# Kernel tuning notes

Hardware: AMD Instinct MI355X
Metric: run time of the kernel (lower is better)

The kernel has to match this reference:

```python
import jax, jax.numpy as jnp
import numpy as np

N = 8192
F_IN = 256
F_OUT = 256
EDGE_P = 0.005  # graph density, avg degree ~41


def setup_inputs() -> dict:
    key = jax.random.key(0)
    k_x, k_adj, k_w, k_phi = jax.random.split(key, 4)
    x = jax.random.normal(k_x, (N, F_IN), dtype=jnp.float32)
    adj = (jax.random.uniform(k_adj, (N, N)) < EDGE_P).astype(jnp.float32)
    stdv_w = 1.0 / np.sqrt(F_OUT)  # torch uses weight.size(1)
    weight = jax.random.uniform(k_w, (F_IN, F_OUT), minval=-stdv_w, maxval=stdv_w, dtype=jnp.float32)
    bias = jnp.zeros((F_OUT,), dtype=jnp.float32)
    stdv_phi = 1.0  # 1/sqrt(phi.size(1)=1)
    phi = jax.random.uniform(k_phi, (2 * F_OUT, 1), minval=-stdv_phi, maxval=stdv_phi, dtype=jnp.float32)
    return {"adj": adj, "x": x, "weight": weight, "bias": bias, "phi": phi}


def reference(adj, x, weight, bias, phi):
    n = x.shape[0]
    H = x @ weight + bias  # [N, F]
    # S[i,j] = phi^T [H_i ; H_j] -> additive decomposition, no [N*N, 2F] concat
    f = H.shape[1]
    s_src = H @ phi[:f, 0]  # [N], contribution of row node i
    s_dst = H @ phi[f:, 0]  # [N], contribution of col node j
    S = s_src[:, None] + s_dst[None, :]  # [N, N]
    mask = (adj + jnp.eye(n, dtype=adj.dtype)) != 0
    S_masked = jnp.where(mask, S, -jnp.inf)
    attn = jax.nn.softmax(S_masked, axis=1)  # diag always unmasked -> no nan rows
    h = attn @ H  # [N, F]
    return jax.nn.leaky_relu(h, negative_slope=0.01)
```

## Files before the change

### kernel.cpp

```cpp
#include <hip/hip_runtime.h>
#include <hip/hip_bf16.h>

typedef __attribute__((ext_vector_type(8))) short short8;
typedef __attribute__((ext_vector_type(4))) float f32x4;

#define N_NODES 8192
#define F 256

static __device__ __forceinline__ unsigned short f2bf(float f) {
    unsigned int u = __builtin_bit_cast(unsigned int, f);
    u += 0x7FFFu + ((u >> 16) & 1u);
    return (unsigned short)(u >> 16);
}
static __device__ __forceinline__ float bf2f(unsigned short h) {
    unsigned int u = ((unsigned int)h) << 16;
    return __builtin_bit_cast(float, u);
}

__global__ __launch_bounds__(256) void k_prep(const float* __restrict__ W,
                                              unsigned short* __restrict__ Wt) {
    int k = blockIdx.x;
    int n = threadIdx.x;
    Wt[n * 256 + k] = f2bf(W[k * 256 + n]);
}

__global__ __launch_bounds__(256) void k_gemm(const float* __restrict__ x,
                                              const float* __restrict__ bias,
                                              const float* __restrict__ phi,
                                              const unsigned short* __restrict__ Wt,
                                              unsigned short* __restrict__ H,
                                              float* __restrict__ s_dst) {
    const int tid  = threadIdx.x;
    const int wave = tid >> 6;
    const int lane = tid & 63;
    const int lrow = lane & 15;
    const int lk   = lane >> 4;
    const int r0   = blockIdx.x * 64 + wave * 16;

    f32x4 acc[16];
#pragma unroll
    for (int n = 0; n < 16; ++n) acc[n] = (f32x4){0.f, 0.f, 0.f, 0.f};

#pragma unroll
    for (int k0 = 0; k0 < 256; k0 += 32) {
        const float* ap = x + (size_t)(r0 + lrow) * 256 + k0 + lk * 8;
        float4 a0 = *(const float4*)ap;
        float4 a1 = *(const float4*)(ap + 4);
        short8 a;
        a[0] = (short)f2bf(a0.x); a[1] = (short)f2bf(a0.y);
        a[2] = (short)f2bf(a0.z); a[3] = (short)f2bf(a0.w);
        a[4] = (short)f2bf(a1.x); a[5] = (short)f2bf(a1.y);
        a[6] = (short)f2bf(a1.z); a[7] = (short)f2bf(a1.w);
#pragma unroll
        for (int n = 0; n < 16; ++n) {
            short8 b = *(const short8*)(Wt + (size_t)(n * 16 + lrow) * 256 + k0 + lk * 8);
            acc[n] = __builtin_amdgcn_mfma_f32_16x16x32_bf16(a, b, acc[n], 0, 0, 0);
        }
    }

    float sd[4] = {0.f, 0.f, 0.f, 0.f};
#pragma unroll
    for (int n = 0; n < 16; ++n) {
        int c = n * 16 + lrow;
        float bv = bias[c];
        float ph = phi[256 + c];
#pragma unroll
        for (int i = 0; i < 4; ++i) {
            int r = r0 + lk * 4 + i;
            float h = acc[n][i] + bv;
            H[(size_t)r * 256 + c] = f2bf(h);
            sd[i] += h * ph;
        }
    }
#pragma unroll
    for (int m = 1; m < 16; m <<= 1) {
#pragma unroll
        for (int i = 0; i < 4; ++i) sd[i] += __shfl_xor(sd[i], m, 64);
    }
    if (lrow == 0) {
#pragma unroll
        for (int i = 0; i < 4; ++i) s_dst[r0 + lk * 4 + i] = sd[i];
    }
}

#define CAP 256
__global__ __launch_bounds__(256) void k_attn(const float* __restrict__ adj,
                                              const unsigned short* __restrict__ H,
                                              const float* __restrict__ s_dst,
                                              float* __restrict__ out) {
    __shared__ int   s_idx[4][CAP];
    __shared__ float s_w[4][CAP];
    __shared__ int   s_cnt[4];

    const int tid  = threadIdx.x;
    const int wave = tid >> 6;
    const int lane = tid & 63;
    const int i    = (blockIdx.x << 2) | wave;

    if (lane == 0) s_cnt[wave] = 0;
    __syncthreads();

    const float4* __restrict__ arow = (const float4*)(adj + (size_t)i * N_NODES);
#pragma unroll 4
    for (int c = 0; c < 32; ++c) {
        int v4 = (c << 6) | lane;
        float4 v = arow[v4];
        int col = v4 << 2;
        float vv[4] = {v.x, v.y, v.z, v.w};
        bool act[4];
        bool any = false;
#pragma unroll
        for (int j = 0; j < 4; ++j) {
            act[j] = (vv[j] != 0.f) || ((col + j) == i);
            any |= act[j];
        }
        if (any) {
#pragma unroll
            for (int j = 0; j < 4; ++j) {
                if (act[j]) {
                    int p = atomicAdd(&s_cnt[wave], 1);
                    if (p < CAP) s_idx[wave][p] = col + j;
                }
            }
        }
    }
    int cnt = min(s_cnt[wave], CAP);

    float mv = -3e38f;
    for (int t = lane; t < cnt; t += 64) {
        float sv = s_dst[s_idx[wave][t]];
        s_w[wave][t] = sv;
        mv = fmaxf(mv, sv);
    }
#pragma unroll
    for (int d = 32; d; d >>= 1) mv = fmaxf(mv, __shfl_xor(mv, d, 64));

    float zv = 0.f;
    for (int t = lane; t < cnt; t += 64) {
        float w = __expf(s_w[wave][t] - mv);
        s_w[wave][t] = w;
        zv += w;
    }
#pragma unroll
    for (int d = 32; d; d >>= 1) zv += __shfl_xor(zv, d, 64);
    const float zinv = 1.0f / zv;

    float a0 = 0.f, a1 = 0.f, a2 = 0.f, a3 = 0.f;
    const unsigned short* __restrict__ hb = H + (lane << 2);
#pragma unroll 4
    for (int t = 0; t < cnt; ++t) {
        int   j = s_idx[wave][t];
        float w = s_w[wave][t];
        short4 hv = *(const short4*)(hb + (size_t)j * F);
        a0 = fmaf(w, bf2f((unsigned short)hv.x), a0);
        a1 = fmaf(w, bf2f((unsigned short)hv.y), a1);
        a2 = fmaf(w, bf2f((unsigned short)hv.z), a2);
        a3 = fmaf(w, bf2f((unsigned short)hv.w), a3);
    }
    float4 o;
    o.x = a0 * zinv; o.y = a1 * zinv; o.z = a2 * zinv; o.w = a3 * zinv;
    o.x = (o.x >= 0.f) ? o.x : 0.01f * o.x;
    o.y = (o.y >= 0.f) ? o.y : 0.01f * o.y;
    o.z = (o.z >= 0.f) ? o.z : 0.01f * o.z;
    o.w = (o.w >= 0.f) ? o.w : 0.01f * o.w;
    *(float4*)(out + (size_t)i * F + (lane << 2)) = o;
}

extern "C" void kernel_launch(void* const* d_in, const int* in_sizes, int n_in,
                              void* d_out, int out_size, void* d_ws, size_t ws_size,
                              hipStream_t stream) {
    const float* adj  = (const float*)d_in[0];
    const float* x    = (const float*)d_in[1];
    const float* W    = (const float*)d_in[2];
    const float* bias = (const float*)d_in[3];
    const float* phi  = (const float*)d_in[4];
    float* out = (float*)d_out;

    char* ws = (char*)d_ws;
    unsigned short* Wt = (unsigned short*)ws;
    unsigned short* H  = (unsigned short*)(ws + (131072));
    float* s_dst       = (float*)(ws + 131072 + 4194304);

    hipLaunchKernelGGL(k_prep, dim3(256),          dim3(256), 0, stream, W, Wt);
    hipLaunchKernelGGL(k_gemm, dim3(N_NODES / 64), dim3(256), 0, stream,
                       x, bias, phi, Wt, H, s_dst);
    hipLaunchKernelGGL(k_attn, dim3(N_NODES / 4),  dim3(256), 0, stream,
                       adj, H, s_dst, out);
}
```

Before: 399.7 us.

## Replace LDS atomic neighbor compaction with ballot prefix and unroll padded gather

Neighbor compaction in the attention kernel now uses wave ballots and mbcnt prefix counts instead of per-element shared-memory atomics, and adjacency rows are read with nontemporal loads. Index and weight are packed into one int2 in shared memory, and the gather loop is padded to a multiple of eight with zero-weight entries so it can be fully unrolled for more outstanding H loads. The CAP overflow guard is dropped, so rows with more than 256 neighbors would write out of bounds.

After: 378.9 us. -5.2%, faster.

```diff
diff --git a/kernel.cpp b/kernel.cpp
--- a/kernel.cpp
+++ b/kernel.cpp
@@ -6,6 +6,7 @@
 
 #define N_NODES 8192
 #define F 256
+#define CAP 256
 
 static __device__ __forceinline__ unsigned short f2bf(float f) {
     unsigned int u = __builtin_bit_cast(unsigned int, f);
@@ -83,79 +84,102 @@
     }
 }
 
-#define CAP 256
 __global__ __launch_bounds__(256) void k_attn(const float* __restrict__ adj,
                                               const unsigned short* __restrict__ H,
                                               const float* __restrict__ s_dst,
                                               float* __restrict__ out) {
-    __shared__ int   s_idx[4][CAP];
-    __shared__ float s_w[4][CAP];
-    __shared__ int   s_cnt[4];
+    __shared__ int  s_idx[4][CAP];
+    __shared__ int2 s_pk[4][CAP];
 
     const int tid  = threadIdx.x;
     const int wave = tid >> 6;
     const int lane = tid & 63;
     const int i    = (blockIdx.x << 2) | wave;
 
-    if (lane == 0) s_cnt[wave] = 0;
-    __syncthreads();
-
-    const float4* __restrict__ arow = (const float4*)(adj + (size_t)i * N_NODES);
-#pragma unroll 4
+    const f32x4* __restrict__ arow = (const f32x4*)(adj + (size_t)i * N_NODES);
+    int cnt = 0;
+#pragma unroll 8
     for (int c = 0; c < 32; ++c) {
         int v4 = (c << 6) | lane;
-        float4 v = arow[v4];
+        f32x4 v = __builtin_nontemporal_load(arow + v4);
         int col = v4 << 2;
-        float vv[4] = {v.x, v.y, v.z, v.w};
-        bool act[4];
-        bool any = false;
-#pragma unroll
-        for (int j = 0; j < 4; ++j) {
-            act[j] = (vv[j] != 0.f) || ((col + j) == i);
-            any |= act[j];
-        }
-        if (any) {
-#pragma unroll
-            for (int j = 0; j < 4; ++j) {
-                if (act[j]) {
-                    int p = atomicAdd(&s_cnt[wave], 1);
-                    if (p < CAP) s_idx[wave][p] = col + j;
-                }
-            }
-        }
-    }
-    int cnt = min(s_cnt[wave], CAP);
+        bool a0 = (v[0] != 0.f) || (col + 0 == i);
+        bool a1 = (v[1] != 0.f) || (col + 1 == i);
+        bool a2 = (v[2] != 0.f) || (col + 2 == i);
+        bool a3 = (v[3] != 0.f) || (col + 3 == i);
+        unsigned long long b0 = __ballot(a0);
+        unsigned long long b1 = __ballot(a1);
+        unsigned long long b2 = __ballot(a2);
+        unsigned long long b3 = __ballot(a3);
+        int base = cnt;
+        if (a0) {
+            int off = __builtin_amdgcn_mbcnt_hi((unsigned)(b0 >> 32),
+                      __builtin_amdgcn_mbcnt_lo((unsigned)b0, 0u));
+            s_idx[wave][base + off] = col;
+        }
+        base += (int)__popcll(b0);
+        if (a1) {
+            int off = __builtin_amdgcn_mbcnt_hi((unsigned)(b1 >> 32),
+                      __builtin_amdgcn_mbcnt_lo((unsigned)b1, 0u));
+            s_idx[wave][base + off] = col + 1;
+        }
+        base += (int)__popcll(b1);
+        if (a2) {
+            int off = __builtin_amdgcn_mbcnt_hi((unsigned)(b2 >> 32),
+                      __builtin_amdgcn_mbcnt_lo((unsigned)b2, 0u));
+            s_idx[wave][base + off] = col + 2;
+        }
+        base += (int)__popcll(b2);
+        if (a3) {
+            int off = __builtin_amdgcn_mbcnt_hi((unsigned)(b3 >> 32),
+                      __builtin_amdgcn_mbcnt_lo((unsigned)b3, 0u));
+            s_idx[wave][base + off] = col + 3;
+        }
+        base += (int)__popcll(b3);
+        cnt = base;
+    }
+    asm volatile("s_waitcnt lgkmcnt(0)" ::: "memory");
 
     float mv = -3e38f;
     for (int t = lane; t < cnt; t += 64) {
-        float sv = s_dst[s_idx[wave][t]];
-        s_w[wave][t] = sv;
+        int j = s_idx[wave][t];
+        float sv = s_dst[j];
+        s_pk[wave][t].x = j;
+        s_pk[wave][t].y = __float_as_int(sv);
         mv = fmaxf(mv, sv);
     }
 #pragma unroll
     for (int d = 32; d; d >>= 1) mv = fmaxf(mv, __shfl_xor(mv, d, 64));
+    asm volatile("s_waitcnt lgkmcnt(0)" ::: "memory");
 
     float zv = 0.f;
     for (int t = lane; t < cnt; t += 64) {
-        float w = __expf(s_w[wave][t] - mv);
-        s_w[wave][t] = w;
+        int2 e = s_pk[wave][t];
+        float w = __expf(__int_as_float(e.y) - mv);
+        s_pk[wave][t].y = __float_as_int(w);
         zv += w;
     }
 #pragma unroll
     for (int d = 32; d; d >>= 1) zv += __shfl_xor(zv, d, 64);
     const float zinv = 1.0f / zv;
 
+    const int P8  = (cnt + 7) & ~7;
+    if (lane < P8 - cnt) s_pk[wave][cnt + lane] = make_int2(i, 0);
+    asm volatile("s_waitcnt lgkmcnt(0)" ::: "memory");
+
     float a0 = 0.f, a1 = 0.f, a2 = 0.f, a3 = 0.f;
     const unsigned short* __restrict__ hb = H + (lane << 2);
-#pragma unroll 4
-    for (int t = 0; t < cnt; ++t) {
-        int   j = s_idx[wave][t];
-        float w = s_w[wave][t];
-        short4 hv = *(const short4*)(hb + (size_t)j * F);
-        a0 = fmaf(w, bf2f((unsigned short)hv.x), a0);
-        a1 = fmaf(w, bf2f((unsigned short)hv.y), a1);
-        a2 = fmaf(w, bf2f((unsigned short)hv.z), a2);
-        a3 = fmaf(w, bf2f((unsigned short)hv.w), a3);
+    for (int t = 0; t < P8; t += 8) {
+#pragma unroll
+        for (int u = 0; u < 8; ++u) {
+            int2 e = s_pk[wave][t + u];
+            float w = __int_as_float(e.y);
+            short4 hv = *(const short4*)(hb + (size_t)e.x * F);
+            a0 = fmaf(w, bf2f((unsigned short)hv.x), a0);
+            a1 = fmaf(w, bf2f((unsigned short)hv.y), a1);
+            a2 = fmaf(w, bf2f((unsigned short)hv.z), a2);
+            a3 = fmaf(w, bf2f((unsigned short)hv.w), a3);
+        }
     }
     float4 o;
     o.x = a0 * zinv; o.y = a1 * zinv; o.z = a2 * zinv; o.w = a3 * zinv;
```
